# Kernel tuning notes

Hardware: AMD Instinct MI355X
Metric: run time of the kernel (lower is better)

Reference implementation:

```python
import jax, jax.numpy as jnp
import numpy as np


def _freq_downsample(x, sf):
    # torch: stack(chunk(dim=2), 4) -> cat(chunk(dim=3), 4) -> mean(-1) -> repeat(1,1,sf,sf)
    # equivalent: mean over the sf x sf grid of contiguous blocks, then tile back.
    B, C, H, W = x.shape
    m = x.reshape(B, C, sf, H // sf, sf, W // sf).mean(axis=(2, 4))
    return jnp.tile(m, (1, 1, sf, sf))


def setup_inputs() -> dict:
    key = jax.random.key(0)
    k1, k2, k3 = jax.random.split(key, 3)
    shape = (4, 3, 256, 256)
    return {
        "STy": jax.random.normal(k1, shape, dtype=jnp.float32),
        "Fk_real": jax.random.normal(k2, shape, dtype=jnp.float32),
        "Fk_imag": jax.random.normal(k3, shape, dtype=jnp.float32),
        "sf": 2,
    }


def _forward(STy, Fk_real, Fk_imag, sf, num_iters=50, alpha=1e-6, gam=0.1):
    fft2 = lambda a: jnp.fft.fft2(a, axes=(-2, -1))
    ifft2 = lambda a: jnp.fft.ifft2(a, axes=(-2, -1))

    Fk = jax.lax.complex(Fk_real, Fk_imag)          # complex64 OTF
    FkC = jnp.conj(Fk)
    Fk2 = Fk_real ** 2 + Fk_imag ** 2               # |Fk|^2, real

    FSTy = fft2(STy)
    Fr = FkC * FSTy / (_freq_downsample(Fk2, sf) + alpha)
    pred = ifft2(Fr).real

    # finite-difference stencils DH = [1,-1] horizontal, DV vertical
    DH = jnp.zeros_like(pred).at[..., 0, 0].set(1.0).at[..., 0, 1].set(-1.0)
    DV = jnp.zeros_like(pred).at[..., 0, 0].set(1.0).at[..., 1, 0].set(-1.0)
    FDH, FDV = fft2(DH), fft2(DV)
    FDHC, FDVC = jnp.conj(FDH), jnp.conj(FDV)
    FD2 = jnp.abs(FDV) ** 2 + jnp.abs(FDH) ** 2 + 1e-8  # real

    # loop-invariant terms (identical math to recomputing each iteration)
    den = _freq_downsample(Fk2 / FD2, sf) + alpha
    FkFSTy = FkC * FSTy

    def body(carry, k):
        pred, x_old, t_old, U1, U2, D1, D2 = carry
        gam_k = gam * jnp.exp2(-k / num_iters)      # gam * 0.5 ** (k/num_iters)
        Fr = FkFSTy + alpha * (FDHC * fft2(U1 - D1) + FDVC * fft2(U2 - D2))
        Fr = (Fr - FkC * _freq_downsample(Fk * Fr / FD2, sf) / den) / (alpha * FD2)
        x_new = ifft2(Fr).real
        t_new = (1.0 + jnp.sqrt(1.0 + 4.0 * t_old ** 2)) / 2.0
        pred = x_new + (t_old - 1.0) / t_new * (x_new - x_old)
        DHr = ifft2(Fr * FDH).real
        DVr = ifft2(Fr * FDV).real
        NU1, NU2 = DHr + D1, DVr + D2
        NU = jnp.sqrt(NU1 ** 2 + NU2 ** 2 + 1e-8)
        A = jnp.maximum(0.0, NU - gam_k) + 1e-8
        A = A / (A + gam_k)                         # soft-threshold magnitude shrink
        U1n, U2n = A * NU1, A * NU2
        return (pred, x_new, t_new, U1n, U2n, D1 + DHr - U1n, D2 + DVr - U2n), None

    carry0 = (pred, pred, jnp.float32(1.0), pred, pred,
              jnp.zeros_like(pred), jnp.zeros_like(pred))
    ks = jnp.arange(num_iters, dtype=jnp.float32)
    (pred, *_), _ = jax.lax.scan(body, carry0, ks)
    return pred


def reference(STy, Fk_real, Fk_imag, sf):
    return _forward(STy, Fk_real, Fk_imag, sf)
```

## Files before the change

### kernel.cpp

```cpp
#include <hip/hip_runtime.h>
#include <math.h>

#define NIMG 12
#define NSZ 256
#define HWSZ 65536
#define NBLK 768

__device__ __forceinline__ void isync(unsigned* flags, int base, int sr, unsigned gen)
{
  __syncthreads();
  int t = threadIdx.x;
  if (t < 64) {
    if (t == 0) {
      __builtin_amdgcn_fence(__ATOMIC_RELEASE, "agent");
      __hip_atomic_store(&flags[base + sr], gen, __ATOMIC_RELAXED, __HIP_MEMORY_SCOPE_AGENT);
    }
    unsigned v;
    do {
      v = __hip_atomic_load(&flags[base + t], __ATOMIC_RELAXED, __HIP_MEMORY_SCOPE_AGENT);
    } while (__any(v < gen));
    __builtin_amdgcn_fence(__ATOMIC_ACQUIRE, "agent");
  }
  __syncthreads();
}

__device__ __forceinline__ void fft256g(float2* A, float2* B, const float2* tw, int lane,
                                        float dir, bool active)
{
  float2* src = A;
  float2* dst = B;
  int m = 1;
#pragma unroll
  for (int s = 0; s < 8; ++s) {
    __syncthreads();
    if (active) {
#pragma unroll
      for (int h = 0; h < 2; ++h) {
        int b = lane + (h << 6);
        int k = b & (m - 1);
        int jm = b - k;
        float2 a = src[b];
        float2 c = src[b + 128];
        float2 w = tw[jm];
        float wr = w.x, wi = dir * w.y;
        float ex = a.x - c.x, ey = a.y - c.y;
        dst[2 * jm + k]     = make_float2(a.x + c.x, a.y + c.y);
        dst[2 * jm + k + m] = make_float2(ex * wr - ey * wi, ex * wi + ey * wr);
      }
    }
    float2* t = src; src = dst; dst = t;
    m <<= 1;
  }
  __syncthreads();
}
__device__ __forceinline__ void fft256(float2* A, float2* B, const float2* tw, int lane, float dir)
{
  fft256g(A, B, tw, lane, dir, true);
}

__device__ __forceinline__ void make_tw(float2* tw, int t)
{
  float s, c;
  sincospif((float)t * (1.0f / 128.0f), &s, &c);
  tw[t] = make_float2(c, s);
}

__device__ __forceinline__ double fdval(const float2* tw, int k)
{
  return 2.0 - 2.0 * (double)tw[k].x;
}

__global__ __launch_bounds__(256, 3) void k_mega(const float* __restrict__ sty,
                                                 const float* __restrict__ fkr,
                                                 const float* __restrict__ fki,
                                                 float2* __restrict__ WG,
                                                 float2* __restrict__ WF,
                                                 float2* __restrict__ FkF,
                                                 float* __restrict__ denq,
                                                 float* D1a, float* D2a,
                                                 float* D1b, float* D2b,
                                                 float* __restrict__ x49,
                                                 float* __restrict__ out,
                                                 float cmom, unsigned* flags)
{
  __shared__ float2 tw[256];
  __shared__ float2 bufA[6][256];
  __shared__ float2 bufB[6][256];
  __shared__ float aL[5][256];
  __shared__ float bL[5][256];
  __shared__ float dsA[2][128];
  __shared__ double2 Ml[2][128];

  int t = threadIdx.x;
  make_tw(tw, t);
  int bid = blockIdx.x;
  int n = bid >> 6;
  int sr = bid & 63;
  int fbase = n << 6;
  int r0 = sr << 2;
  int j0 = sr << 1;
  int w = t >> 6, lane = t & 63;
  const float sc = 1.0f / 65536.0f;
  int gcw = j0 + (w & 1) + ((w >> 1) << 7);
  unsigned gen = 0;

  {
    const float* src = sty + (size_t)n * HWSZ + (size_t)(r0 + w) * NSZ;
#pragma unroll
    for (int q = 0; q < 4; ++q) { int j = lane + (q << 6); bufA[w][j] = make_float2(src[j], 0.f); }
    fft256(bufA[w], bufB[w], tw, lane, -1.f);
    float2* dst = WG + (size_t)n * HWSZ + (size_t)(r0 + w) * NSZ;
#pragma unroll
    for (int q = 0; q < 4; ++q) { int j = lane + (q << 6); dst[j] = bufA[w][j]; }
  }
  isync(flags, fbase, sr, ++gen);

  {
    float2* WGn = WG + (size_t)n * HWSZ;
#pragma unroll
    for (int q = 0; q < 4; ++q) { int u = lane + (q << 6); bufA[w][u] = WGn[(size_t)u * NSZ + gcw]; }
    fft256(bufA[w], bufB[w], tw, lane, -1.f);
#pragma unroll
    for (int c = 0; c < 4; ++c) {
      int u = t;
      int gc = j0 + (c & 1) + ((c >> 1) << 7);
      size_t idx = (size_t)n * HWSZ + (size_t)u * NSZ + gc;
      float kr = fkr[idx], ki = fki[idx];
      float2 f = bufA[c][u];
      float2 kf = make_float2(kr * f.x + ki * f.y, kr * f.y - ki * f.x);
      FkF[idx] = kf;
      bufA[c][u] = kf;
    }
    __syncthreads();
    {
      int u0 = t & 127, p = t >> 7;
      double s1 = 0.0, s2 = 0.0;
#pragma unroll
      for (int s = 0; s < 4; ++s) {
        int u = u0 + ((s & 1) << 7);
        int c = p + ((s >> 1) << 1);
        int gc = j0 + (c & 1) + ((c >> 1) << 7);
        size_t idx = (size_t)n * HWSZ + (size_t)u * NSZ + gc;
        double kr = fkr[idx], ki = fki[idx];
        double k2 = kr * kr + ki * ki;
        double fd2 = fdval(tw, u) + fdval(tw, gc) + 1e-8;
        s1 += k2;
        s2 += k2 / fd2;
      }
      denq[(size_t)n * 16384 + (size_t)u0 * 128 + (j0 + p)] = (float)(s2 * 0.25 + 1e-6);
      dsA[p][u0] = (float)(s1 * 0.25 + 1e-6);
    }
    __syncthreads();
#pragma unroll
    for (int c = 0; c < 4; ++c) {
      int u = t;
      float d = dsA[c & 1][u & 127];
      float2 kf = bufA[c][u];
      bufA[c][u] = make_float2(kf.x / d, kf.y / d);
    }
    fft256(bufA[w], bufB[w], tw, lane, +1.f);
    float2* WFn = WF + (size_t)n * HWSZ;
#pragma unroll
    for (int q = 0; q < 4; ++q) { int u = lane + (q << 6); WFn[(size_t)u * NSZ + gcw] = bufA[w][u]; }
  }
  isync(flags, fbase, sr, ++gen);

  for (int k = 0; k < 50; ++k) {
    float gamp = (k >= 1) ? (float)(0.1 * exp2(-(double)(k - 1) / 50.0)) : 0.f;
    const float *D1p, *D2p; float *D1w, *D2w;
    if (k & 1) { D1p = D1a; D2p = D2a; D1w = D1b; D2w = D2b; }
    else       { D1p = D1b; D2p = D2b; D1w = D1a; D2w = D2a; }

    {
      int gr = (r0 + w - 1) & 255;
      const float2* srcW = WF + (size_t)n * HWSZ + (size_t)gr * NSZ;
#pragma unroll
      for (int q = 0; q < 4; ++q) { int j = lane + (q << 6); bufA[w][j] = srcW[j]; }
      fft256(bufA[w], bufB[w], tw, lane, +1.f);
    }
    {
      bool act = (w < 2);
      int e = 4 + (w & 1);
      int gr = (r0 + e - 1) & 255;
      if (act) {
        const float2* srcW = WF + (size_t)n * HWSZ + (size_t)gr * NSZ;
#pragma unroll
        for (int q = 0; q < 4; ++q) { int j = lane + (q << 6); bufA[e][j] = srcW[j]; }
      }
      fft256g(bufA[e], bufB[e], tw, lane, +1.f, act);
    }
    for (int e = 1; e <= 5; ++e) {
      int gr = (r0 + e - 1) & 255;
      int j = t, jm1 = (j - 1) & 255;
      float xc = bufA[e][j].x * sc;
      size_t idx = (size_t)n * HWSZ + (size_t)gr * NSZ + j;
      if (k == 49 && e <= 4) x49[idx] = xc;
      float a, b;
      if (k == 0) {
        a = xc; b = xc;
      } else {
        float xl = bufA[e][jm1].x * sc;
        float xu = bufA[e - 1][j].x * sc;
        float dhr = xc - xl;
        float dvr = xc - xu;
        float d1 = D1p[idx], d2 = D2p[idx];
        float nu1 = dhr + d1, nu2 = dvr + d2;
        float nu = sqrtf(nu1 * nu1 + nu2 * nu2 + 1e-8f);
        float A = fmaxf(0.f, nu - gamp) + 1e-8f;
        A = A / (A + gamp);
        float u1 = A * nu1, u2 = A * nu2;
        float d1v = d1 + dhr - u1;
        float d2v = d2 + dvr - u2;
        if (e <= 4) { D1w[idx] = d1v; D2w[idx] = d2v; }
        a = u1 - d1v; b = u2 - d2v;
      }
      aL[e - 1][j] = a;
      bL[e - 1][j] = b;
    }
    __syncthreads();
    {
#pragma unroll
      for (int q = 0; q < 4; ++q) {
        int j = lane + (q << 6);
        int jp1 = (j + 1) & 255;
        float g = aL[w][j] - aL[w][jp1] + bL[w][j] - bL[w + 1][j];
        bufA[w][j] = make_float2(g, 0.f);
      }
      fft256(bufA[w], bufB[w], tw, lane, -1.f);
      float2* dst = WG + (size_t)n * HWSZ + (size_t)(r0 + w) * NSZ;
#pragma unroll
      for (int q = 0; q < 4; ++q) { int j = lane + (q << 6); dst[j] = bufA[w][j]; }
    }
    isync(flags, fbase, sr, ++gen);

    {
      float2* WGn = WG + (size_t)n * HWSZ;
#pragma unroll
      for (int q = 0; q < 4; ++q) { int u = lane + (q << 6); bufA[w][u] = WGn[(size_t)u * NSZ + gcw]; }
      fft256(bufA[w], bufB[w], tw, lane, -1.f);
#pragma unroll
      for (int c = 0; c < 4; ++c) {
        int u = t;
        int gc = j0 + (c & 1) + ((c >> 1) << 7);
        size_t idx = (size_t)n * HWSZ + (size_t)u * NSZ + gc;
        float2 kf = FkF[idx];
        float2 fg = bufA[c][u];
        bufA[c][u] = make_float2(kf.x + 1e-6f * fg.x, kf.y + 1e-6f * fg.y);
      }
      __syncthreads();
      {
        int u0 = t & 127, p = t >> 7;
        double sx = 0.0, sy = 0.0;
#pragma unroll
        for (int s = 0; s < 4; ++s) {
          int u = u0 + ((s & 1) << 7);
          int c = p + ((s >> 1) << 1);
          int gc = j0 + (c & 1) + ((c >> 1) << 7);
          size_t idx = (size_t)n * HWSZ + (size_t)u * NSZ + gc;
          float2 f1 = bufA[c][u];
          double kr = fkr[idx], ki = fki[idx];
          double fd2 = fdval(tw, u) + fdval(tw, gc) + 1e-8;
          sx += (kr * (double)f1.x - ki * (double)f1.y) / fd2;
          sy += (kr * (double)f1.y + ki * (double)f1.x) / fd2;
        }
        Ml[p][u0] = make_double2(sx * 0.25, sy * 0.25);
      }
      __syncthreads();
#pragma unroll
      for (int c = 0; c < 4; ++c) {
        int u = t;
        int gc = j0 + (c & 1) + ((c >> 1) << 7);
        size_t idx = (size_t)n * HWSZ + (size_t)u * NSZ + gc;
        float2 f1 = bufA[c][u];
        double2 m = Ml[c & 1][u & 127];
        double den = (double)denq[(size_t)n * 16384 + (size_t)(u & 127) * 128 + (j0 + (c & 1))];
        double kr = fkr[idx], ki = fki[idx];
        double px = (kr * m.x + ki * m.y) / den;
        double py = (kr * m.y - ki * m.x) / den;
        double fd2 = fdval(tw, u) + fdval(tw, gc) + 1e-8;
        double s2 = 1.0 / (1e-6 * fd2);
        bufA[c][u] = make_float2((float)(((double)f1.x - px) * s2),
                                 (float)(((double)f1.y - py) * s2));
      }
      fft256(bufA[w], bufB[w], tw, lane, +1.f);
      float2* WFn = WF + (size_t)n * HWSZ;
#pragma unroll
      for (int q = 0; q < 4; ++q) { int u = lane + (q << 6); WFn[(size_t)u * NSZ + gcw] = bufA[w][u]; }
    }
    isync(flags, fbase, sr, ++gen);
  }

  {
    const float2* srcW = WF + (size_t)n * HWSZ + (size_t)(r0 + w) * NSZ;
#pragma unroll
    for (int q = 0; q < 4; ++q) { int j = lane + (q << 6); bufA[w][j] = srcW[j]; }
    fft256(bufA[w], bufB[w], tw, lane, +1.f);
    size_t base = (size_t)n * HWSZ + (size_t)(r0 + w) * NSZ;
#pragma unroll
    for (int q = 0; q < 4; ++q) {
      int j = lane + (q << 6);
      float v = bufA[w][j].x * sc;
      out[base + j] = v + cmom * (v - x49[base + j]);
    }
  }
}

__global__ __launch_bounds__(256) void k_rowfwd_sty(const float* __restrict__ sty,
                                                    float2* __restrict__ Wb)
{
  __shared__ float2 tw[256];
  __shared__ float2 bufA[4][256];
  __shared__ float2 bufB[4][256];
  int t = threadIdx.x;
  make_tw(tw, t);
  int n = blockIdx.x >> 6;
  int r0 = (blockIdx.x & 63) << 2;
  int w = t >> 6, lane = t & 63;
  const float* src = sty + (size_t)n * HWSZ + (size_t)(r0 + w) * NSZ;
#pragma unroll
  for (int q = 0; q < 4; ++q) { int j = lane + (q << 6); bufA[w][j] = make_float2(src[j], 0.f); }
  fft256(bufA[w], bufB[w], tw, lane, -1.f);
  float2* dst = Wb + (size_t)n * HWSZ + (size_t)(r0 + w) * NSZ;
#pragma unroll
  for (int q = 0; q < 4; ++q) { int j = lane + (q << 6); dst[j] = bufA[w][j]; }
}

__global__ __launch_bounds__(256) void k_colsetup(float2* __restrict__ Wb,
                                                  float2* __restrict__ FkF,
                                                  const float* __restrict__ fkr,
                                                  const float* __restrict__ fki,
                                                  float* __restrict__ denq)
{
  __shared__ float2 tw[256];
  __shared__ float2 bufA[4][256];
  __shared__ float2 bufB[4][256];
  __shared__ float dsA[2][128];
  int t = threadIdx.x;
  make_tw(tw, t);
  int n = blockIdx.x >> 6;
  int j0 = (blockIdx.x & 63) << 1;
  int w = t >> 6, lane = t & 63;
  int gcw = j0 + (w & 1) + ((w >> 1) << 7);
  float2* Wn = Wb + (size_t)n * HWSZ;
#pragma unroll
  for (int q = 0; q < 4; ++q) { int u = lane + (q << 6); bufA[w][u] = Wn[(size_t)u * NSZ + gcw]; }
  fft256(bufA[w], bufB[w], tw, lane, -1.f);
#pragma unroll
  for (int c = 0; c < 4; ++c) {
    int u = t;
    int gc = j0 + (c & 1) + ((c >> 1) << 7);
    size_t idx = (size_t)n * HWSZ + (size_t)u * NSZ + gc;
    float kr = fkr[idx], ki = fki[idx];
    float2 f = bufA[c][u];
    float2 kf = make_float2(kr * f.x + ki * f.y, kr * f.y - ki * f.x);
    FkF[idx] = kf;
    bufA[c][u] = kf;
  }
  __syncthreads();
  {
    int u0 = t & 127, p = t >> 7;
    double s1 = 0.0, s2 = 0.0;
#pragma unroll
    for (int s = 0; s < 4; ++s) {
      int u = u0 + ((s & 1) << 7);
      int c = p + ((s >> 1) << 1);
      int gc = j0 + (c & 1) + ((c >> 1) << 7);
      size_t idx = (size_t)n * HWSZ + (size_t)u * NSZ + gc;
      double kr = fkr[idx], ki = fki[idx];
      double k2 = kr * kr + ki * ki;
      double fd2 = fdval(tw, u) + fdval(tw, gc) + 1e-8;
      s1 += k2;
      s2 += k2 / fd2;
    }
    denq[(size_t)n * 16384 + (size_t)u0 * 128 + (j0 + p)] = (float)(s2 * 0.25 + 1e-6);
    dsA[p][u0] = (float)(s1 * 0.25 + 1e-6);
  }
  __syncthreads();
#pragma unroll
  for (int c = 0; c < 4; ++c) {
    int u = t;
    float d = dsA[c & 1][u & 127];
    float2 kf = bufA[c][u];
    bufA[c][u] = make_float2(kf.x / d, kf.y / d);
  }
  fft256(bufA[w], bufB[w], tw, lane, +1.f);
#pragma unroll
  for (int q = 0; q < 4; ++q) { int u = lane + (q << 6); Wn[(size_t)u * NSZ + gcw] = bufA[w][u]; }
}

__global__ __launch_bounds__(256) void k_spatial_rowfwd(const float* __restrict__ x,
                                                        const float* __restrict__ D1p,
                                                        const float* __restrict__ D2p,
                                                        float* __restrict__ D1n,
                                                        float* __restrict__ D2n,
                                                        float2* __restrict__ Wb,
                                                        float gamp, int firstIter)
{
  __shared__ float2 tw[256];
  __shared__ float aL[5][256];
  __shared__ float bL[5][256];
  __shared__ float2 bufA[4][256];
  __shared__ float2 bufB[4][256];
  int t = threadIdx.x;
  make_tw(tw, t);
  int n = blockIdx.x >> 6;
  int r0 = (blockIdx.x & 63) << 2;
  const float* xn = x + (size_t)n * HWSZ;
  for (int rr = 0; rr < 5; ++rr) {
    int i = (r0 + rr) & 255;
    int im1 = (i - 1) & 255;
    int j = t;
    int jm1 = (j - 1) & 255;
    float xc = xn[(size_t)i * NSZ + j];
    float a, b;
    if (firstIter) {
      a = xc; b = xc;
    } else {
      float dhr = xc - xn[(size_t)i * NSZ + jm1];
      float dvr = xc - xn[(size_t)im1 * NSZ + j];
      size_t idx = (size_t)n * HWSZ + (size_t)i * NSZ + j;
      float d1 = D1p[idx], d2 = D2p[idx];
      float nu1 = dhr + d1, nu2 = dvr + d2;
      float nu = sqrtf(nu1 * nu1 + nu2 * nu2 + 1e-8f);
      float A = fmaxf(0.f, nu - gamp) + 1e-8f;
      A = A / (A + gamp);
      float u1 = A * nu1, u2 = A * nu2;
      float d1v = d1 + dhr - u1;
      float d2v = d2 + dvr - u2;
      if (rr < 4) { D1n[idx] = d1v; D2n[idx] = d2v; }
      a = u1 - d1v; b = u2 - d2v;
    }
    aL[rr][j] = a;
    bL[rr][j] = b;
  }
  __syncthreads();
  int w = t >> 6, lane = t & 63;
#pragma unroll
  for (int q = 0; q < 4; ++q) {
    int j = lane + (q << 6);
    int jp1 = (j + 1) & 255;
    float g = aL[w][j] - aL[w][jp1] + bL[w][j] - bL[w + 1][j];
    bufA[w][j] = make_float2(g, 0.f);
  }
  fft256(bufA[w], bufB[w], tw, lane, -1.f);
  float2* dst = Wb + (size_t)n * HWSZ + (size_t)(r0 + w) * NSZ;
#pragma unroll
  for (int q = 0; q < 4; ++q) { int j = lane + (q << 6); dst[j] = bufA[w][j]; }
}

__global__ __launch_bounds__(256) void k_colphase(float2* __restrict__ Wb,
                                                  const float2* __restrict__ FkF,
                                                  const float* __restrict__ fkr,
                                                  const float* __restrict__ fki,
                                                  const float* __restrict__ denq)
{
  __shared__ float2 tw[256];
  __shared__ float2 bufA[4][256];
  __shared__ float2 bufB[4][256];
  __shared__ double2 Ml[2][128];
  int t = threadIdx.x;
  make_tw(tw, t);
  int n = blockIdx.x >> 6;
  int j0 = (blockIdx.x & 63) << 1;
  int w = t >> 6, lane = t & 63;
  int gcw = j0 + (w & 1) + ((w >> 1) << 7);
  float2* Wn = Wb + (size_t)n * HWSZ;
#pragma unroll
  for (int q = 0; q < 4; ++q) { int u = lane + (q << 6); bufA[w][u] = Wn[(size_t)u * NSZ + gcw]; }
  fft256(bufA[w], bufB[w], tw, lane, -1.f);
#pragma unroll
  for (int c = 0; c < 4; ++c) {
    int u = t;
    int gc = j0 + (c & 1) + ((c >> 1) << 7);
    size_t idx = (size_t)n * HWSZ + (size_t)u * NSZ + gc;
    float2 kf = FkF[idx];
    float2 fg = bufA[c][u];
    bufA[c][u] = make_float2(kf.x + 1e-6f * fg.x, kf.y + 1e-6f * fg.y);
  }
  __syncthreads();
  {
    int u0 = t & 127, p = t >> 7;
    double sx = 0.0, sy = 0.0;
#pragma unroll
    for (int s = 0; s < 4; ++s) {
      int u = u0 + ((s & 1) << 7);
      int c = p + ((s >> 1) << 1);
      int gc = j0 + (c & 1) + ((c >> 1) << 7);
      size_t idx = (size_t)n * HWSZ + (size_t)u * NSZ + gc;
      float2 f1 = bufA[c][u];
      double kr = fkr[idx], ki = fki[idx];
      double fd2 = fdval(tw, u) + fdval(tw, gc) + 1e-8;
      sx += (kr * (double)f1.x - ki * (double)f1.y) / fd2;
      sy += (kr * (double)f1.y + ki * (double)f1.x) / fd2;
    }
    Ml[p][u0] = make_double2(sx * 0.25, sy * 0.25);
  }
  __syncthreads();
#pragma unroll
  for (int c = 0; c < 4; ++c) {
    int u = t;
    int gc = j0 + (c & 1) + ((c >> 1) << 7);
    size_t idx = (size_t)n * HWSZ + (size_t)u * NSZ + gc;
    float2 f1 = bufA[c][u];
    double2 m = Ml[c & 1][u & 127];
    double den = (double)denq[(size_t)n * 16384 + (size_t)(u & 127) * 128 + (j0 + (c & 1))];
    double kr = fkr[idx], ki = fki[idx];
    double px = (kr * m.x + ki * m.y) / den;
    double py = (kr * m.y - ki * m.x) / den;
    double fd2 = fdval(tw, u) + fdval(tw, gc) + 1e-8;
    double s2 = 1.0 / (1e-6 * fd2);
    bufA[c][u] = make_float2((float)(((double)f1.x - px) * s2),
                             (float)(((double)f1.y - py) * s2));
  }
  fft256(bufA[w], bufB[w], tw, lane, +1.f);
#pragma unroll
  for (int q = 0; q < 4; ++q) { int u = lane + (q << 6); Wn[(size_t)u * NSZ + gcw] = bufA[w][u]; }
}

__global__ __launch_bounds__(256) void k_rowinv(const float2* __restrict__ Wb,
                                                float* __restrict__ xout,
                                                const float* __restrict__ xold,
                                                float* __restrict__ pred,
                                                float cmom, int isLast)
{
  __shared__ float2 tw[256];
  __shared__ float2 bufA[4][256];
  __shared__ float2 bufB[4][256];
  int t = threadIdx.x;
  make_tw(tw, t);
  int n = blockIdx.x >> 6;
  int r0 = (blockIdx.x & 63) << 2;
  int w = t >> 6, lane = t & 63;
  const float2* src = Wb + (size_t)n * HWSZ + (size_t)(r0 + w) * NSZ;
#pragma unroll
  for (int q = 0; q < 4; ++q) { int j = lane + (q << 6); bufA[w][j] = src[j]; }
  fft256(bufA[w], bufB[w], tw, lane, +1.f);
  size_t base = (size_t)n * HWSZ + (size_t)(r0 + w) * NSZ;
#pragma unroll
  for (int q = 0; q < 4; ++q) {
    int j = lane + (q << 6);
    float v = bufA[w][j].x * (1.0f / 65536.0f);
    xout[base + j] = v;
    if (isLast) pred[base + j] = v + cmom * (v - xold[base + j]);
  }
}

extern "C" void kernel_launch(void* const* d_in, const int* in_sizes, int n_in,
                              void* d_out, int out_size, void* d_ws, size_t ws_size,
                              hipStream_t stream)
{
  (void)in_sizes; (void)n_in; (void)out_size; (void)ws_size;
  const float* STy = (const float*)d_in[0];
  const float* fkr = (const float*)d_in[1];
  const float* fki = (const float*)d_in[2];
  float* out = (float*)d_out;

  char* p = (char*)d_ws;
  const size_t cplx = (size_t)NIMG * HWSZ * sizeof(float2);
  const size_t realb = (size_t)NIMG * HWSZ * sizeof(float);
  float2* WG  = (float2*)p; p += cplx;
  float2* WF  = (float2*)p; p += cplx;
  float2* FkF = (float2*)p; p += cplx;
  float* denq = (float*)p;  p += (size_t)NIMG * 16384 * sizeof(float);
  float* D1a = (float*)p;   p += realb;
  float* D2a = (float*)p;   p += realb;
  float* D1b = (float*)p;   p += realb;
  float* D2b = (float*)p;   p += realb;
  float* xA  = (float*)p;   p += realb;
  float* xB  = (float*)p;   p += realb;
  unsigned* flags = (unsigned*)p; p += 4096;

  double t_old = 1.0, cm = 0.0;
  for (int k = 0; k < 50; ++k) {
    double t_new = (1.0 + sqrt(1.0 + 4.0 * t_old * t_old)) * 0.5;
    if (k == 49) cm = (t_old - 1.0) / t_new;
    t_old = t_new;
  }

  int maxb = 0;
  hipError_t oe = hipOccupancyMaxActiveBlocksPerMultiprocessor(&maxb, k_mega, 256, 0);
  bool coop = (oe == hipSuccess && maxb >= 3);

  hipMemsetAsync(D1a, 0, 2 * realb, stream);

  dim3 grid(NBLK), blk(256);
  if (coop) {
    hipMemsetAsync(flags, 0, 4096, stream);
    k_mega<<<grid, blk, 0, stream>>>(STy, fkr, fki, WG, WF, FkF, denq,
                                     D1a, D2a, D1b, D2b, xA, out, (float)cm, flags);
  } else {
    float2* Wb = WG;
    float* x0 = xA; float* x1 = xB;
    k_rowfwd_sty<<<grid, blk, 0, stream>>>(STy, Wb);
    k_colsetup<<<grid, blk, 0, stream>>>(Wb, FkF, fkr, fki, denq);
    k_rowinv<<<grid, blk, 0, stream>>>(Wb, x0, x0, out, 0.f, 0);
    double to = 1.0;
    for (int k = 0; k < 50; ++k) {
      float gamp = (k >= 1) ? (float)(0.1 * exp2(-(double)(k - 1) / 50.0)) : 0.f;
      const float* xk = (k & 1) ? x1 : x0;
      float* xn = (k & 1) ? x0 : x1;
      const float* D1p = (k & 1) ? D1a : D1b;
      const float* D2p = (k & 1) ? D2a : D2b;
      float* D1w = (k & 1) ? D1b : D1a;
      float* D2w = (k & 1) ? D2b : D2a;
      k_spatial_rowfwd<<<grid, blk, 0, stream>>>(xk, D1p, D2p, D1w, D2w, Wb, gamp, (k == 0) ? 1 : 0);
      k_colphase<<<grid, blk, 0, stream>>>(Wb, FkF, fkr, fki, denq);
      double tn = (1.0 + sqrt(1.0 + 4.0 * to * to)) * 0.5;
      int isLast = (k == 49) ? 1 : 0;
      float cmom = (float)((to - 1.0) / tn);
      k_rowinv<<<grid, blk, 0, stream>>>(Wb, xn, xk, out, isLast ? cmom : 0.f, isLast);
      to = tn;
    }
  }
}
```

Measured before the change: 2.485 ms.

## Keep per-block state in LDS and tile spectral buffers for coalesced column access

The persistent mega-kernel now keeps Fk, Fk·FSTy, the denominator and the block-owned D1/D2 rows in shared memory across all iterations, instead of re-reading them from global memory each step. Only the halo D row is exchanged through a small double-buffered global array. WG/WF use a tiled layout so each block's four columns sit contiguously, which makes the column-pass loads and stores coalesced, and block IDs are remapped to spread images across XCDs. The cost is much higher LDS use (scratch aliased over several arrays), which may threaten the three-blocks-per-CU occupancy that the cooperative path requires.

```diff
diff --git a/kernel.cpp b/kernel.cpp
--- a/kernel.cpp
+++ b/kernel.cpp
@@ -5,6 +5,13 @@
 #define NSZ 256
 #define HWSZ 65536
 #define NBLK 768
+
+__device__ __forceinline__ size_t widx(int n, int u, int j)
+{
+  int tile = (j & 127) >> 1;
+  int slot = (j & 1) + ((j >> 7) << 1);
+  return ((((size_t)n << 6) + tile) << 10) + ((size_t)u << 2) + slot;
+}
 
 __device__ __forceinline__ void isync(unsigned* flags, int base, int sr, unsigned gen)
 {
@@ -75,61 +82,63 @@
                                                  const float* __restrict__ fki,
                                                  float2* __restrict__ WG,
                                                  float2* __restrict__ WF,
-                                                 float2* __restrict__ FkF,
-                                                 float* __restrict__ denq,
-                                                 float* D1a, float* D2a,
-                                                 float* D1b, float* D2b,
+                                                 float* __restrict__ Dh,
                                                  float* __restrict__ x49,
                                                  float* __restrict__ out,
                                                  float cmom, unsigned* flags)
 {
   __shared__ float2 tw[256];
   __shared__ float2 bufA[6][256];
-  __shared__ float2 bufB[6][256];
-  __shared__ float aL[5][256];
-  __shared__ float bL[5][256];
-  __shared__ float dsA[2][128];
-  __shared__ double2 Ml[2][128];
+  __shared__ float2 scrB[6][256];
+  __shared__ float2 fkL[4][256];
+  __shared__ float2 kfL[4][256];
+  __shared__ float  dnL[256];
+  __shared__ float  D1L[4][256];
+  __shared__ float  D2L[4][256];
+
+  float*   aL   = (float*)scrB;
+  float*   bL   = ((float*)scrB) + 5 * 256;
+  double2* Ml   = (double2*)scrB;
+  float*   dsAp = (float*)scrB;
 
   int t = threadIdx.x;
   make_tw(tw, t);
-  int bid = blockIdx.x;
-  int n = bid >> 6;
-  int sr = bid & 63;
+  int slot = ((blockIdx.x & 7) * 96) + (blockIdx.x >> 3);
+  int n = slot >> 6;
+  int sr = slot & 63;
   int fbase = n << 6;
   int r0 = sr << 2;
   int j0 = sr << 1;
   int w = t >> 6, lane = t & 63;
   const float sc = 1.0f / 65536.0f;
-  int gcw = j0 + (w & 1) + ((w >> 1) << 7);
+  size_t cb = ((((size_t)n << 6) + sr) << 10);
   unsigned gen = 0;
 
   {
     const float* src = sty + (size_t)n * HWSZ + (size_t)(r0 + w) * NSZ;
 #pragma unroll
     for (int q = 0; q < 4; ++q) { int j = lane + (q << 6); bufA[w][j] = make_float2(src[j], 0.f); }
-    fft256(bufA[w], bufB[w], tw, lane, -1.f);
-    float2* dst = WG + (size_t)n * HWSZ + (size_t)(r0 + w) * NSZ;
-#pragma unroll
-    for (int q = 0; q < 4; ++q) { int j = lane + (q << 6); dst[j] = bufA[w][j]; }
+    fft256(bufA[w], scrB[w], tw, lane, -1.f);
+#pragma unroll
+    for (int q = 0; q < 4; ++q) { int j = lane + (q << 6); WG[widx(n, r0 + w, j)] = bufA[w][j]; }
+#pragma unroll
+    for (int c = 0; c < 4; ++c) {
+      int gc = j0 + (c & 1) + ((c >> 1) << 7);
+      size_t idx = (size_t)n * HWSZ + (size_t)t * NSZ + gc;
+      fkL[c][t] = make_float2(fkr[idx], fki[idx]);
+    }
   }
   isync(flags, fbase, sr, ++gen);
 
   {
-    float2* WGn = WG + (size_t)n * HWSZ;
-#pragma unroll
-    for (int q = 0; q < 4; ++q) { int u = lane + (q << 6); bufA[w][u] = WGn[(size_t)u * NSZ + gcw]; }
-    fft256(bufA[w], bufB[w], tw, lane, -1.f);
+#pragma unroll
+    for (int q = 0; q < 4; ++q) { int u = lane + (q << 6); bufA[w][u] = WG[cb + (u << 2) + w]; }
+    fft256(bufA[w], scrB[w], tw, lane, -1.f);
 #pragma unroll
     for (int c = 0; c < 4; ++c) {
-      int u = t;
-      int gc = j0 + (c & 1) + ((c >> 1) << 7);
-      size_t idx = (size_t)n * HWSZ + (size_t)u * NSZ + gc;
-      float kr = fkr[idx], ki = fki[idx];
-      float2 f = bufA[c][u];
-      float2 kf = make_float2(kr * f.x + ki * f.y, kr * f.y - ki * f.x);
-      FkF[idx] = kf;
-      bufA[c][u] = kf;
+      float2 K = fkL[c][t];
+      float2 f = bufA[c][t];
+      kfL[c][t] = make_float2(K.x * f.x + K.y * f.y, K.x * f.y - K.y * f.x);
     }
     __syncthreads();
     {
@@ -140,82 +149,81 @@
         int u = u0 + ((s & 1) << 7);
         int c = p + ((s >> 1) << 1);
         int gc = j0 + (c & 1) + ((c >> 1) << 7);
-        size_t idx = (size_t)n * HWSZ + (size_t)u * NSZ + gc;
-        double kr = fkr[idx], ki = fki[idx];
+        double kr = fkL[c][u].x, ki = fkL[c][u].y;
         double k2 = kr * kr + ki * ki;
         double fd2 = fdval(tw, u) + fdval(tw, gc) + 1e-8;
         s1 += k2;
         s2 += k2 / fd2;
       }
-      denq[(size_t)n * 16384 + (size_t)u0 * 128 + (j0 + p)] = (float)(s2 * 0.25 + 1e-6);
-      dsA[p][u0] = (float)(s1 * 0.25 + 1e-6);
+      dnL[u0 * 2 + p] = (float)(s2 * 0.25 + 1e-6);
+      dsAp[p * 128 + u0] = (float)(s1 * 0.25 + 1e-6);
     }
     __syncthreads();
 #pragma unroll
     for (int c = 0; c < 4; ++c) {
-      int u = t;
-      float d = dsA[c & 1][u & 127];
-      float2 kf = bufA[c][u];
-      bufA[c][u] = make_float2(kf.x / d, kf.y / d);
-    }
-    fft256(bufA[w], bufB[w], tw, lane, +1.f);
-    float2* WFn = WF + (size_t)n * HWSZ;
-#pragma unroll
-    for (int q = 0; q < 4; ++q) { int u = lane + (q << 6); WFn[(size_t)u * NSZ + gcw] = bufA[w][u]; }
+      float d = dsAp[(c & 1) * 128 + (t & 127)];
+      float2 kf = kfL[c][t];
+      bufA[c][t] = make_float2(kf.x / d, kf.y / d);
+    }
+    fft256(bufA[w], scrB[w], tw, lane, +1.f);
+#pragma unroll
+    for (int q = 0; q < 4; ++q) { int u = lane + (q << 6); WF[cb + (u << 2) + w] = bufA[w][u]; }
   }
   isync(flags, fbase, sr, ++gen);
 
   for (int k = 0; k < 50; ++k) {
     float gamp = (k >= 1) ? (float)(0.1 * exp2(-(double)(k - 1) / 50.0)) : 0.f;
-    const float *D1p, *D2p; float *D1w, *D2w;
-    if (k & 1) { D1p = D1a; D2p = D2a; D1w = D1b; D2w = D2b; }
-    else       { D1p = D1b; D2p = D2b; D1w = D1a; D2w = D2a; }
 
     {
       int gr = (r0 + w - 1) & 255;
-      const float2* srcW = WF + (size_t)n * HWSZ + (size_t)gr * NSZ;
-#pragma unroll
-      for (int q = 0; q < 4; ++q) { int j = lane + (q << 6); bufA[w][j] = srcW[j]; }
-      fft256(bufA[w], bufB[w], tw, lane, +1.f);
+#pragma unroll
+      for (int q = 0; q < 4; ++q) { int j = lane + (q << 6); bufA[w][j] = WF[widx(n, gr, j)]; }
+      fft256(bufA[w], scrB[w], tw, lane, +1.f);
     }
     {
       bool act = (w < 2);
       int e = 4 + (w & 1);
       int gr = (r0 + e - 1) & 255;
       if (act) {
-        const float2* srcW = WF + (size_t)n * HWSZ + (size_t)gr * NSZ;
-#pragma unroll
-        for (int q = 0; q < 4; ++q) { int j = lane + (q << 6); bufA[e][j] = srcW[j]; }
-      }
-      fft256g(bufA[e], bufB[e], tw, lane, +1.f, act);
-    }
-    for (int e = 1; e <= 5; ++e) {
-      int gr = (r0 + e - 1) & 255;
-      int j = t, jm1 = (j - 1) & 255;
-      float xc = bufA[e][j].x * sc;
-      size_t idx = (size_t)n * HWSZ + (size_t)gr * NSZ + j;
-      if (k == 49 && e <= 4) x49[idx] = xc;
-      float a, b;
-      if (k == 0) {
-        a = xc; b = xc;
-      } else {
-        float xl = bufA[e][jm1].x * sc;
-        float xu = bufA[e - 1][j].x * sc;
-        float dhr = xc - xl;
-        float dvr = xc - xu;
-        float d1 = D1p[idx], d2 = D2p[idx];
-        float nu1 = dhr + d1, nu2 = dvr + d2;
-        float nu = sqrtf(nu1 * nu1 + nu2 * nu2 + 1e-8f);
-        float A = fmaxf(0.f, nu - gamp) + 1e-8f;
-        A = A / (A + gamp);
-        float u1 = A * nu1, u2 = A * nu2;
-        float d1v = d1 + dhr - u1;
-        float d2v = d2 + dvr - u2;
-        if (e <= 4) { D1w[idx] = d1v; D2w[idx] = d2v; }
-        a = u1 - d1v; b = u2 - d2v;
-      }
-      aL[e - 1][j] = a;
-      bL[e - 1][j] = b;
+#pragma unroll
+        for (int q = 0; q < 4; ++q) { int j = lane + (q << 6); bufA[e][j] = WF[widx(n, gr, j)]; }
+      }
+      fft256g(bufA[e], scrB[e], tw, lane, +1.f, act);
+    }
+    {
+      int jm1 = (t - 1) & 255;
+      size_t hR = (((size_t)n << 6) + ((sr + 1) & 63)) << 9;
+      size_t hW = (((size_t)n << 6) + sr) << 9;
+      const float* DhP = Dh + (size_t)((k + 1) & 1) * (NBLK * 512);
+      float* DhW = Dh + (size_t)(k & 1) * (NBLK * 512);
+      for (int e = 1; e <= 5; ++e) {
+        int gr = (r0 + e - 1) & 255;
+        float xc = bufA[e][t].x * sc;
+        if (k == 49 && e <= 4) x49[(size_t)n * HWSZ + (size_t)gr * NSZ + t] = xc;
+        float a, b;
+        if (k == 0) {
+          a = xc; b = xc;
+          if (e <= 4) { D1L[e - 1][t] = 0.f; D2L[e - 1][t] = 0.f; }
+        } else {
+          float dhr = xc - bufA[e][jm1].x * sc;
+          float dvr = xc - bufA[e - 1][t].x * sc;
+          float d1, d2;
+          if (e <= 4) { d1 = D1L[e - 1][t]; d2 = D2L[e - 1][t]; }
+          else        { d1 = DhP[hR + t];   d2 = DhP[hR + 256 + t]; }
+          float nu1 = dhr + d1, nu2 = dvr + d2;
+          float nu = sqrtf(nu1 * nu1 + nu2 * nu2 + 1e-8f);
+          float A = fmaxf(0.f, nu - gamp) + 1e-8f;
+          A = A / (A + gamp);
+          float u1 = A * nu1, u2 = A * nu2;
+          float d1v = d1 + dhr - u1;
+          float d2v = d2 + dvr - u2;
+          if (e <= 4) { D1L[e - 1][t] = d1v; D2L[e - 1][t] = d2v; }
+          if (e == 1) { DhW[hW + t] = d1v; DhW[hW + 256 + t] = d2v; }
+          a = u1 - d1v; b = u2 - d2v;
+        }
+        aL[(e - 1) * 256 + t] = a;
+        bL[(e - 1) * 256 + t] = b;
+      }
     }
     __syncthreads();
     {
@@ -223,29 +231,24 @@
       for (int q = 0; q < 4; ++q) {
         int j = lane + (q << 6);
         int jp1 = (j + 1) & 255;
-        float g = aL[w][j] - aL[w][jp1] + bL[w][j] - bL[w + 1][j];
+        float g = aL[w * 256 + j] - aL[w * 256 + jp1] + bL[w * 256 + j] - bL[(w + 1) * 256 + j];
         bufA[w][j] = make_float2(g, 0.f);
       }
-      fft256(bufA[w], bufB[w], tw, lane, -1.f);
-      float2* dst = WG + (size_t)n * HWSZ + (size_t)(r0 + w) * NSZ;
-#pragma unroll
-      for (int q = 0; q < 4; ++q) { int j = lane + (q << 6); dst[j] = bufA[w][j]; }
+      fft256(bufA[w], scrB[w], tw, lane, -1.f);
+#pragma unroll
+      for (int q = 0; q < 4; ++q) { int j = lane + (q << 6); WG[widx(n, r0 + w, j)] = bufA[w][j]; }
     }
     isync(flags, fbase, sr, ++gen);
 
     {
-      float2* WGn = WG + (size_t)n * HWSZ;
-#pragma unroll
-      for (int q = 0; q < 4; ++q) { int u = lane + (q << 6); bufA[w][u] = WGn[(size_t)u * NSZ + gcw]; }
-      fft256(bufA[w], bufB[w], tw, lane, -1.f);
+#pragma unroll
+      for (int q = 0; q < 4; ++q) { int u = lane + (q << 6); bufA[w][u] = WG[cb + (u << 2) + w]; }
+      fft256(bufA[w], scrB[w], tw, lane, -1.f);
 #pragma unroll
       for (int c = 0; c < 4; ++c) {
-        int u = t;
-        int gc = j0 + (c & 1) + ((c >> 1) << 7);
-        size_t idx = (size_t)n * HWSZ + (size_t)u * NSZ + gc;
-        float2 kf = FkF[idx];
-        float2 fg = bufA[c][u];
-        bufA[c][u] = make_float2(kf.x + 1e-6f * fg.x, kf.y + 1e-6f * fg.y);
+        float2 kf = kfL[c][t];
+        float2 fg = bufA[c][t];
+        bufA[c][t] = make_float2(kf.x + 1e-6f * fg.x, kf.y + 1e-6f * fg.y);
       }
       __syncthreads();
       {
@@ -256,25 +259,23 @@
           int u = u0 + ((s & 1) << 7);
           int c = p + ((s >> 1) << 1);
           int gc = j0 + (c & 1) + ((c >> 1) << 7);
-          size_t idx = (size_t)n * HWSZ + (size_t)u * NSZ + gc;
           float2 f1 = bufA[c][u];
-          double kr = fkr[idx], ki = fki[idx];
+          double kr = fkL[c][u].x, ki = fkL[c][u].y;
           double fd2 = fdval(tw, u) + fdval(tw, gc) + 1e-8;
           sx += (kr * (double)f1.x - ki * (double)f1.y) / fd2;
           sy += (kr * (double)f1.y + ki * (double)f1.x) / fd2;
         }
-        Ml[p][u0] = make_double2(sx * 0.25, sy * 0.25);
+        Ml[p * 128 + u0] = make_double2(sx * 0.25, sy * 0.25);
       }
       __syncthreads();
 #pragma unroll
       for (int c = 0; c < 4; ++c) {
         int u = t;
         int gc = j0 + (c & 1) + ((c >> 1) << 7);
-        size_t idx = (size_t)n * HWSZ + (size_t)u * NSZ + gc;
         float2 f1 = bufA[c][u];
-        double2 m = Ml[c & 1][u & 127];
-        double den = (double)denq[(size_t)n * 16384 + (size_t)(u & 127) * 128 + (j0 + (c & 1))];
-        double kr = fkr[idx], ki = fki[idx];
+        double2 m = Ml[(c & 1) * 128 + (u & 127)];
+        double den = (double)dnL[(u & 127) * 2 + (c & 1)];
+        double kr = fkL[c][u].x, ki = fkL[c][u].y;
         double px = (kr * m.x + ki * m.y) / den;
         double py = (kr * m.y - ki * m.x) / den;
         double fd2 = fdval(tw, u) + fdval(tw, gc) + 1e-8;
@@ -282,20 +283,19 @@
         bufA[c][u] = make_float2((float)(((double)f1.x - px) * s2),
                                  (float)(((double)f1.y - py) * s2));
       }
-      fft256(bufA[w], bufB[w], tw, lane, +1.f);
-      float2* WFn = WF + (size_t)n * HWSZ;
-#pragma unroll
-      for (int q = 0; q < 4; ++q) { int u = lane + (q << 6); WFn[(size_t)u * NSZ + gcw] = bufA[w][u]; }
+      fft256(bufA[w], scrB[w], tw, lane, +1.f);
+#pragma unroll
+      for (int q = 0; q < 4; ++q) { int u = lane + (q << 6); WF[cb + (u << 2) + w] = bufA[w][u]; }
     }
     isync(flags, fbase, sr, ++gen);
   }
 
   {
-    const float2* srcW = WF + (size_t)n * HWSZ + (size_t)(r0 + w) * NSZ;
-#pragma unroll
-    for (int q = 0; q < 4; ++q) { int j = lane + (q << 6); bufA[w][j] = srcW[j]; }
-    fft256(bufA[w], bufB[w], tw, lane, +1.f);
-    size_t base = (size_t)n * HWSZ + (size_t)(r0 + w) * NSZ;
+    int gr = r0 + w;
+#pragma unroll
+    for (int q = 0; q < 4; ++q) { int j = lane + (q << 6); bufA[w][j] = WF[widx(n, gr, j)]; }
+    fft256(bufA[w], scrB[w], tw, lane, +1.f);
+    size_t base = (size_t)n * HWSZ + (size_t)gr * NSZ;
 #pragma unroll
     for (int q = 0; q < 4; ++q) {
       int j = lane + (q << 6);
@@ -568,6 +568,7 @@
   float* D2b = (float*)p;   p += realb;
   float* xA  = (float*)p;   p += realb;
   float* xB  = (float*)p;   p += realb;
+  float* Dh  = (float*)p;   p += (size_t)2 * NBLK * 512 * sizeof(float);
   unsigned* flags = (unsigned*)p; p += 4096;
 
   double t_old = 1.0, cm = 0.0;
@@ -581,14 +582,13 @@
   hipError_t oe = hipOccupancyMaxActiveBlocksPerMultiprocessor(&maxb, k_mega, 256, 0);
   bool coop = (oe == hipSuccess && maxb >= 3);
 
-  hipMemsetAsync(D1a, 0, 2 * realb, stream);
-
   dim3 grid(NBLK), blk(256);
   if (coop) {
+    hipMemsetAsync(Dh, 0, (size_t)2 * NBLK * 512 * sizeof(float), stream);
     hipMemsetAsync(flags, 0, 4096, stream);
-    k_mega<<<grid, blk, 0, stream>>>(STy, fkr, fki, WG, WF, FkF, denq,
-                                     D1a, D2a, D1b, D2b, xA, out, (float)cm, flags);
+    k_mega<<<grid, blk, 0, stream>>>(STy, fkr, fki, WG, WF, Dh, xA, out, (float)cm, flags);
   } else {
+    hipMemsetAsync(D1a, 0, 2 * realb, stream);
     float2* Wb = WG;
     float* x0 = xA; float* x1 = xB;
     k_rowfwd_sty<<<grid, blk, 0, stream>>>(STy, Wb);
```

Result: no change. 2.498 ms (+0.5%).
